# Kernel tuning notes

Measured on AMD Instinct MI355X. Metric: run time of the kernel, lower is better.

Reference implementation:

```python
import jax, jax.numpy as jnp
import numpy as np
import math

B, S, H = 2, 2048, 1024
NH, HD = 16, 64
MAX_SCALE = 4


def setup_inputs() -> dict:
    key = jax.random.key(0)
    ks = jax.random.split(key, 8)
    s = 0.02
    return {
        "x": jax.random.normal(ks[0], (B, S, H), dtype=jnp.float32),
        "Wqkv": jax.random.normal(ks[1], (H, 3 * H), dtype=jnp.float32) * s,
        "bqkv": jnp.zeros((3 * H,), dtype=jnp.float32),
        "Wout": jax.random.normal(ks[2], (H, H), dtype=jnp.float32) * s,
        "bout": jnp.zeros((H,), dtype=jnp.float32),
        "Wscale": jax.random.normal(ks[3], (H, MAX_SCALE), dtype=jnp.float32) * s,
        "bscale": jnp.zeros((MAX_SCALE,), dtype=jnp.float32),
    }


def reference(x, Wqkv, bqkv, Wout, bout, Wscale, bscale):
    b, s, h = x.shape
    inv_sqrt_hd = 1.0 / math.sqrt(HD)
    # qkv projection -> [3, b, nh, s, hd]
    qkv = (x @ Wqkv + bqkv).reshape(b, s, 3, NH, HD).transpose(2, 0, 3, 1, 4)
    q, k, v = qkv[0], qkv[1], qkv[2]
    # per-token soft weights over scales [b, s, max_scale]
    scale_weights = jax.nn.softmax(x @ Wscale + bscale, axis=-1)
    out = jnp.zeros((b, NH, s, HD), dtype=x.dtype)
    for scale_idx in range(MAX_SCALE):
        dilation = 2 ** scale_idx
        kd = k[:, :, ::dilation]  # strided (dilated) gather of keys
        vd = v[:, :, ::dilation]
        scores = jnp.einsum("bhqd,bhkd->bhqk", q, kd) * inv_sqrt_hd
        attn = jax.nn.softmax(scores, axis=-1)
        o = jnp.einsum("bhqk,bhkd->bhqd", attn, vd)
        w = scale_weights[:, :, scale_idx][:, None, :, None]  # [b,1,s,1]
        out = out + o * w
    out = out.transpose(0, 2, 1, 3).reshape(b, s, h)
    return out @ Wout + bout
```

## Files before the change

kernel.cpp:

```cpp
#include <hip/hip_runtime.h>
#include <stdint.h>

typedef unsigned short u16;
typedef __attribute__((ext_vector_type(8))) __bf16 bf8v;
typedef __attribute__((ext_vector_type(4))) float f4v;
typedef __attribute__((ext_vector_type(16))) float f16v;
typedef __attribute__((ext_vector_type(4))) uint32_t u32x4;

#define BB 2
#define SS 2048
#define HH 1024

#define OFF_Q   0u
#define OFF_K0  8388608u
#define OFF_V0  24117248u
#define OFF_WQT 39845888u
#define OFF_WOT 46137344u
#define OFF_XB  48234496u
#define OFF_SCW 56623104u

__device__ __forceinline__ u16 f2bf(float f) {
    union { float f; uint32_t u; } v; v.f = f;
    uint32_t r = v.u + 0x7fffu + ((v.u >> 16) & 1u);
    return (u16)(r >> 16);
}
__device__ __forceinline__ uint32_t pk2(float a, float b) {
    return (uint32_t)f2bf(a) | ((uint32_t)f2bf(b) << 16);
}
__device__ __forceinline__ uint32_t pkt2(float a, float b) {
    union { float f; uint32_t u; } x, y; x.f = a; y.f = b;
    return (x.u >> 16) | (y.u & 0xffff0000u);
}
__device__ __forceinline__ bf8v u2b(uint4 v) {
    union { uint4 u; bf8v b; } x; x.u = v; return x.b;
}

__global__ __launch_bounds__(256) void xconv_kernel(const float* __restrict__ x,
                                                    u16* __restrict__ xb) {
    size_t t = (size_t)blockIdx.x * 256 + threadIdx.x;
    float4 v = *(const float4*)&x[t * 4];
    uint2 pk; pk.x = pk2(v.x, v.y); pk.y = pk2(v.z, v.w);
    *(uint2*)&xb[t * 4] = pk;
}

__global__ __launch_bounds__(256) void wconv_kernel(const float* __restrict__ W,
                                                    u16* __restrict__ Wt,
                                                    int N, int K) {
    __shared__ float tile[64][69];
    const int tid = threadIdx.x;
    const int n0 = blockIdx.x * 64, k0 = blockIdx.y * 64;
    const int r = tid >> 4, c4 = (tid & 15) * 4;
#pragma unroll
    for (int it = 0; it < 4; it++) {
        float4 v = *(const float4*)&W[(size_t)(k0 + it * 16 + r) * N + n0 + c4];
        tile[it * 16 + r][c4 + 0] = v.x; tile[it * 16 + r][c4 + 1] = v.y;
        tile[it * 16 + r][c4 + 2] = v.z; tile[it * 16 + r][c4 + 3] = v.w;
    }
    __syncthreads();
#pragma unroll
    for (int it = 0; it < 4; it++) {
        int n = it * 16 + r;
        uint2 pk;
        pk.x = pk2(tile[c4 + 0][n], tile[c4 + 1][n]);
        pk.y = pk2(tile[c4 + 2][n], tile[c4 + 3][n]);
        *(uint2*)&Wt[(size_t)(n0 + n) * K + k0 + c4] = pk;
    }
}

__global__ __launch_bounds__(256) void scale_kernel(const float* __restrict__ x,
                                                    const float* __restrict__ Wscale,
                                                    const float* __restrict__ bscale,
                                                    float* __restrict__ scw) {
    const int lane = threadIdx.x & 63;
    const int wid  = threadIdx.x >> 6;
    const int row  = blockIdx.x * 4 + wid;
    float a0 = 0.f, a1 = 0.f, a2 = 0.f, a3 = 0.f;
    for (int i = 0; i < 16; i++) {
        int hh = lane + i * 64;
        float xs = x[(size_t)row * HH + hh];
        float4 wv = *(const float4*)&Wscale[hh * 4];
        a0 += xs * wv.x; a1 += xs * wv.y; a2 += xs * wv.z; a3 += xs * wv.w;
    }
    for (int off = 1; off < 64; off <<= 1) {
        a0 += __shfl_xor(a0, off); a1 += __shfl_xor(a1, off);
        a2 += __shfl_xor(a2, off); a3 += __shfl_xor(a3, off);
    }
    if (lane == 0) {
        a0 += bscale[0]; a1 += bscale[1]; a2 += bscale[2]; a3 += bscale[3];
        float mx = fmaxf(fmaxf(a0, a1), fmaxf(a2, a3));
        float e0 = __expf(a0 - mx), e1 = __expf(a1 - mx);
        float e2 = __expf(a2 - mx), e3 = __expf(a3 - mx);
        float inv = 1.f / (e0 + e1 + e2 + e3);
        float4 o = {e0 * inv, e1 * inv, e2 * inv, e3 * inv};
        *(float4*)&scw[(size_t)row * 4] = o;
    }
}

template<int MODE>
__global__ __launch_bounds__(256) void gemm_bt(const u16* __restrict__ A,
                                               const u16* __restrict__ Bt,
                                               const float* __restrict__ bias,
                                               void* __restrict__ Cp,
                                               int N, int K) {
    __shared__ __align__(16) u16 At[128 * 40];
    __shared__ __align__(16) u16 Btl[128 * 40];
    const int tid  = threadIdx.x;
    const int lane = tid & 63;
    const int wid  = tid >> 6;
    const int l15  = lane & 15;
    const int quad = lane >> 4;
    const int wm = wid & 1, wn = wid >> 1;
    const int m0 = blockIdx.y * 128;
    const int n0 = blockIdx.x * 128;
    const int srow = tid >> 2;
    const int sc8  = (tid & 3) * 8;

    f4v acc[4][4];
#pragma unroll
    for (int i = 0; i < 4; i++)
#pragma unroll
        for (int j = 0; j < 4; j++) acc[i][j] = (f4v){0.f, 0.f, 0.f, 0.f};

    uint4 pa0 = *(const uint4*)(A  + (size_t)(m0 + srow) * K + sc8);
    uint4 pa1 = *(const uint4*)(A  + (size_t)(m0 + srow + 64) * K + sc8);
    uint4 pb0 = *(const uint4*)(Bt + (size_t)(n0 + srow) * K + sc8);
    uint4 pb1 = *(const uint4*)(Bt + (size_t)(n0 + srow + 64) * K + sc8);

    for (int kc = 0; kc < K; kc += 32) {
        __syncthreads();
        *(uint4*)&At[srow * 40 + sc8]         = pa0;
        *(uint4*)&At[(srow + 64) * 40 + sc8]  = pa1;
        *(uint4*)&Btl[srow * 40 + sc8]        = pb0;
        *(uint4*)&Btl[(srow + 64) * 40 + sc8] = pb1;
        __syncthreads();
        if (kc + 32 < K) {
            pa0 = *(const uint4*)(A  + (size_t)(m0 + srow) * K + kc + 32 + sc8);
            pa1 = *(const uint4*)(A  + (size_t)(m0 + srow + 64) * K + kc + 32 + sc8);
            pb0 = *(const uint4*)(Bt + (size_t)(n0 + srow) * K + kc + 32 + sc8);
            pb1 = *(const uint4*)(Bt + (size_t)(n0 + srow + 64) * K + kc + 32 + sc8);
        }
        bf8v af[4], bf[4];
#pragma unroll
        for (int t = 0; t < 4; t++) {
            af[t] = *(const bf8v*)&At[(wm * 64 + t * 16 + l15) * 40 + quad * 8];
            bf[t] = *(const bf8v*)&Btl[(wn * 64 + t * 16 + l15) * 40 + quad * 8];
        }
#pragma unroll
        for (int ti = 0; ti < 4; ti++)
#pragma unroll
            for (int tj = 0; tj < 4; tj++)
                acc[ti][tj] = __builtin_amdgcn_mfma_f32_16x16x32_bf16(af[ti], bf[tj], acc[ti][tj], 0, 0, 0);
    }

    if (MODE == 0) {
#pragma unroll
        for (int ti = 0; ti < 4; ti++)
#pragma unroll
            for (int tj = 0; tj < 4; tj++)
#pragma unroll
                for (int r = 0; r < 4; r++) {
                    int m = m0 + wm * 64 + ti * 16 + quad * 4 + r;
                    int n = n0 + wn * 64 + tj * 16 + l15;
                    ((float*)Cp)[(size_t)m * N + n] = acc[ti][tj][r] + bias[n];
                }
    } else {
        char* ws = (char*)Cp;
        u16* Qd = (u16*)ws;
        u16* K0 = (u16*)(ws + OFF_K0);
        u16* V0 = (u16*)(ws + OFF_V0);
        const int region = n0 >> 10;
        if (region == 0) {
#pragma unroll
            for (int ti = 0; ti < 4; ti++)
#pragma unroll
                for (int tj = 0; tj < 4; tj++)
#pragma unroll
                    for (int r = 0; r < 4; r++) {
                        int m = m0 + wm * 64 + ti * 16 + quad * 4 + r;
                        int n = n0 + wn * 64 + tj * 16 + l15;
                        Qd[(size_t)m * 1024 + n] = f2bf(acc[ti][tj][r] + bias[n]);
                    }
        } else if (region == 1) {
#pragma unroll
            for (int ti = 0; ti < 4; ti++)
#pragma unroll
                for (int tj = 0; tj < 4; tj++) {
                    int n  = n0 + wn * 64 + tj * 16 + l15;
                    int nk = n - 1024;
                    int h = nk >> 6, hd = nk & 63;
#pragma unroll
                    for (int r = 0; r < 4; r++) {
                        int m = m0 + wm * 64 + ti * 16 + quad * 4 + r;
                        int bb = m >> 11, tok = m & 2047;
                        int bh = bb * 16 + h;
                        u16 bv = f2bf((acc[ti][tj][r] + bias[n]) * 0.18033688f);
                        K0[((size_t)bh * 2048 + tok) * 64 + hd] = bv;
                    }
                }
        } else {
#pragma unroll
            for (int ti = 0; ti < 4; ti++)
#pragma unroll
                for (int tj = 0; tj < 4; tj++) {
                    int n  = n0 + wn * 64 + tj * 16 + l15;
                    int nv = n - 2048;
                    int h = nv >> 6, hd = nv & 63;
                    int tokb = m0 + wm * 64 + ti * 16 + quad * 4;
                    int bb = tokb >> 11, tok = tokb & 2047;
                    int bh = bb * 16 + h;
                    float v0 = acc[ti][tj][0] + bias[n];
                    float v1 = acc[ti][tj][1] + bias[n];
                    float v2 = acc[ti][tj][2] + bias[n];
                    float v3 = acc[ti][tj][3] + bias[n];
                    u16 c0 = f2bf(v0), c1 = f2bf(v1), c2 = f2bf(v2), c3 = f2bf(v3);
                    uint2 pk;
                    pk.x = (uint32_t)c0 | ((uint32_t)c1 << 16);
                    pk.y = (uint32_t)c2 | ((uint32_t)c3 << 16);
                    int tokp = (tok & ~15) | ((tok & 4) << 1) | ((tok & 8) >> 1);
                    *(uint2*)&V0[((size_t)bh * 64 + hd) * 2048 + tokp] = pk;
                }
        }
    }
}

#define PITER(C, KA, BUFC, BUFN)                                               \
    {                                                                          \
        const int c = (C);                                                     \
        f16v sa = sinit;                                                       \
        sa = __builtin_amdgcn_mfma_f32_32x32x16_bf16(u2b(KA[0]), qf[0], sa, 0, 0, 0); \
        sa = __builtin_amdgcn_mfma_f32_32x32x16_bf16(u2b(KA[1]), qf[1], sa, 0, 0, 0); \
        sa = __builtin_amdgcn_mfma_f32_32x32x16_bf16(u2b(KA[2]), qf[2], sa, 0, 0, 0); \
        sa = __builtin_amdgcn_mfma_f32_32x32x16_bf16(u2b(KA[3]), qf[3], sa, 0, 0, 0); \
        if (c + 2 < 64) {                                                      \
            _Pragma("unroll")                                                  \
            for (int ks = 0; ks < 4; ks++)                                     \
                KA[ks] = *(const uint4*)(Kb + (size_t)((c + 2) * 32 + l31) * 64 + ks * 16 + half * 8); \
        }                                                                      \
        if (c + 1 < 64) *(uint4*)&(BUFN)[sr * 40 + svk8] = vr;                 \
        if (c + 2 < 64) vr = *(const uint4*)(Vb0 + (size_t)sr * 2048 + (c + 2) * 32 + svk8); \
        uint32_t F0, F1, F2, F3, F4, F5, F6, F7;                               \
        {                                                                      \
            float x0, x1, x2, x3;                                              \
            x0 = exp2f(sa[0]);  x1 = exp2f(sa[1]);                             \
            x2 = exp2f(sa[2]);  x3 = exp2f(sa[3]);                             \
            F0 = pkt2(x0, x1); F1 = pkt2(x2, x3);                              \
            x0 = exp2f(sa[4]);  x1 = exp2f(sa[5]);                             \
            x2 = exp2f(sa[6]);  x3 = exp2f(sa[7]);                             \
            F2 = pkt2(x0, x1); F3 = pkt2(x2, x3);                              \
            x0 = exp2f(sa[8]);  x1 = exp2f(sa[9]);                             \
            x2 = exp2f(sa[10]); x3 = exp2f(sa[11]);                            \
            F4 = pkt2(x0, x1); F5 = pkt2(x2, x3);                              \
            x0 = exp2f(sa[12]); x1 = exp2f(sa[13]);                            \
            x2 = exp2f(sa[14]); x3 = exp2f(sa[15]);                            \
            F6 = pkt2(x0, x1); F7 = pkt2(x2, x3);                              \
        }                                                                      \
        uu p0; p0.u = (u32x4){F0, F1, F2, F3};                                 \
        uu p1; p1.u = (u32x4){F4, F5, F6, F7};                                 \
        bf8v va00 = *(const bf8v*)&(BUFC)[l31 * 40 + half * 8];                \
        oacc[0] = __builtin_amdgcn_mfma_f32_32x32x16_bf16(va00, p0.b, oacc[0], 0, 0, 0); \
        bf8v va01 = *(const bf8v*)&(BUFC)[l31 * 40 + 16 + half * 8];           \
        oacc[0] = __builtin_amdgcn_mfma_f32_32x32x16_bf16(va01, p1.b, oacc[0], 0, 0, 0); \
        bf8v va10 = *(const bf8v*)&(BUFC)[(32 + l31) * 40 + half * 8];         \
        oacc[1] = __builtin_amdgcn_mfma_f32_32x32x16_bf16(va10, p0.b, oacc[1], 0, 0, 0); \
        bf8v va11 = *(const bf8v*)&(BUFC)[(32 + l31) * 40 + 16 + half * 8];    \
        oacc[1] = __builtin_amdgcn_mfma_f32_32x32x16_bf16(va11, p1.b, oacc[1], 0, 0, 0); \
        __syncthreads();                                                       \
    }

__global__ __launch_bounds__(256, 2) void attn_kernel(const char* __restrict__ ws) {
    __shared__ __align__(16) u16 smem[5120];
    u16* Vt0 = smem;
    u16* Vt1 = smem + 2560;

    const u16* Qd    = (const u16*)(ws + OFF_Q);
    const float* scw = (const float*)(ws + OFF_SCW);
    u16* attnb       = (u16*)(ws + OFF_Q);

    const int tid  = threadIdx.x;
    const int lane = tid & 63;
    const int wid  = tid >> 6;
    const int l31  = lane & 31;
    const int half = lane >> 5;

    const int f   = blockIdx.x + 16 * blockIdx.y + 256 * blockIdx.z;
    const int xcd = f & 7, jj = f >> 3;
    const int grp = xcd * 4 + (jj >> 4);
    const int qt  = jj & 15;
    const int b = grp >> 4, h = grp & 15;
    const int q  = qt * 128 + wid * 32 + l31;
    const int bh = b * 16 + h;

    const int sr   = tid >> 2;
    const int svk8 = (tid & 3) * 8;

    bf8v qf[4];
#pragma unroll
    for (int ks = 0; ks < 4; ks++)
        qf[ks] = *(const bf8v*)(Qd + (size_t)(b * SS + q) * 1024 + h * 64 + ks * 16 + half * 8);

    const u16* Kb  = (const u16*)(ws + OFF_K0) + (size_t)bh * (2048 * 64);
    const u16* Vb0 = (const u16*)(ws + OFF_V0) + (size_t)bh * (64 * 2048);

    union uu { u32x4 u; bf8v b; };

    float ls0 = 0.f, ls1 = 0.f, ls2 = 0.f, ls3 = 0.f;
    uint4 kp[4], kq[4];
#pragma unroll
    for (int ks = 0; ks < 4; ks++) {
        kp[ks] = *(const uint4*)(Kb + (size_t)l31 * 64 + ks * 16 + half * 8);
        kq[ks] = *(const uint4*)(Kb + (size_t)(32 + l31) * 64 + ks * 16 + half * 8);
    }
    for (int c = 0; c < 64; c += 2) {
        f16v sA = {0,0,0,0,0,0,0,0,0,0,0,0,0,0,0,0};
        f16v sB = {0,0,0,0,0,0,0,0,0,0,0,0,0,0,0,0};
#pragma unroll
        for (int ks = 0; ks < 4; ks++) {
            sA = __builtin_amdgcn_mfma_f32_32x32x16_bf16(u2b(kp[ks]), qf[ks], sA, 0, 0, 0);
            sB = __builtin_amdgcn_mfma_f32_32x32x16_bf16(u2b(kq[ks]), qf[ks], sB, 0, 0, 0);
        }
        if (c + 2 < 64) {
#pragma unroll
            for (int ks = 0; ks < 4; ks++)
                kp[ks] = *(const uint4*)(Kb + (size_t)((c + 2) * 32 + l31) * 64 + ks * 16 + half * 8);
#pragma unroll
            for (int ks = 0; ks < 4; ks++)
                kq[ks] = *(const uint4*)(Kb + (size_t)((c + 3) * 32 + l31) * 64 + ks * 16 + half * 8);
        }
#pragma unroll
        for (int g = 0; g < 4; g++) {
            float x0 = exp2f(sA[4 * g + 0]);
            float x1 = exp2f(sA[4 * g + 1]);
            float x2 = exp2f(sA[4 * g + 2]);
            float x3 = exp2f(sA[4 * g + 3]);
            ls0 += (x0 + x1) + (x2 + x3);
            ls1 += x0 + x2;
            ls2 += x0;
            if (!half) ls3 += x0;
        }
#pragma unroll
        for (int g = 0; g < 4; g++) {
            float x0 = exp2f(sB[4 * g + 0]);
            float x1 = exp2f(sB[4 * g + 1]);
            float x2 = exp2f(sB[4 * g + 2]);
            float x3 = exp2f(sB[4 * g + 3]);
            ls0 += (x0 + x1) + (x2 + x3);
            ls1 += x0 + x2;
            ls2 += x0;
            if (!half) ls3 += x0;
        }
    }
    ls0 += __shfl_xor(ls0, 32);
    ls1 += __shfl_xor(ls1, 32);
    ls2 += __shfl_xor(ls2, 32);
    ls3 += __shfl_xor(ls3, 32);

    float4 sw = *(const float4*)&scw[(size_t)(b * SS + q) * 4];
    float m0v = sw.x / ls0;
    float m2v = m0v + sw.y / ls1;
    float mAv = m2v + sw.z / ls2;
    float mBv = mAv + sw.w / ls3;
    float lmO = log2f(m0v);
    float lmE = log2f(m2v);
    float lmZ = log2f(half ? mAv : mBv);
    f16v sinit;
#pragma unroll
    for (int g = 0; g < 4; g++) {
        sinit[4 * g + 0] = lmZ; sinit[4 * g + 1] = lmO;
        sinit[4 * g + 2] = lmE; sinit[4 * g + 3] = lmO;
    }

    f16v oacc[2];
#pragma unroll
    for (int ht = 0; ht < 2; ht++)
#pragma unroll
        for (int r = 0; r < 16; r++) oacc[ht][r] = 0.f;

    *(uint4*)&Vt0[sr * 40 + svk8] = *(const uint4*)(Vb0 + (size_t)sr * 2048 + svk8);
    uint4 vr = *(const uint4*)(Vb0 + (size_t)sr * 2048 + 32 + svk8);
#pragma unroll
    for (int ks = 0; ks < 4; ks++) {
        kp[ks] = *(const uint4*)(Kb + (size_t)l31 * 64 + ks * 16 + half * 8);
        kq[ks] = *(const uint4*)(Kb + (size_t)(32 + l31) * 64 + ks * 16 + half * 8);
    }
    __syncthreads();

    for (int cc = 0; cc < 64; cc += 2) {
        PITER(cc,     kp, Vt0, Vt1)
        PITER(cc + 1, kq, Vt1, Vt0)
    }

    const size_t base = (size_t)(b * SS + q) * 1024 + h * 64;
#pragma unroll
    for (int ht = 0; ht < 2; ht++)
#pragma unroll
        for (int g = 0; g < 4; g++) {
            uint2 pk;
            pk.x = pk2(oacc[ht][g * 4 + 0], oacc[ht][g * 4 + 1]);
            pk.y = pk2(oacc[ht][g * 4 + 2], oacc[ht][g * 4 + 3]);
            *(uint2*)&attnb[base + ht * 32 + g * 8 + half * 4] = pk;
        }
}

extern "C" void kernel_launch(void* const* d_in, const int* in_sizes, int n_in,
                              void* d_out, int out_size, void* d_ws, size_t ws_size,
                              hipStream_t stream) {
    const float* x      = (const float*)d_in[0];
    const float* Wqkv   = (const float*)d_in[1];
    const float* bqkv   = (const float*)d_in[2];
    const float* Wout   = (const float*)d_in[3];
    const float* bout   = (const float*)d_in[4];
    const float* Wscale = (const float*)d_in[5];
    const float* bscale = (const float*)d_in[6];
    float* out = (float*)d_out;

    char* ws = (char*)d_ws;
    u16*   wqt   = (u16*)(ws + OFF_WQT);
    u16*   wot   = (u16*)(ws + OFF_WOT);
    u16*   xb    = (u16*)(ws + OFF_XB);
    u16*   attnb = (u16*)(ws + OFF_Q);
    float* scw   = (float*)(ws + OFF_SCW);

    xconv_kernel<<<dim3(4096), dim3(256), 0, stream>>>(x, xb);
    wconv_kernel<<<dim3(48, 16), dim3(256), 0, stream>>>(Wqkv, wqt, 3072, 1024);
    wconv_kernel<<<dim3(16, 16), dim3(256), 0, stream>>>(Wout, wot, 1024, 1024);
    scale_kernel<<<dim3(1024), dim3(256), 0, stream>>>(x, Wscale, bscale, scw);
    gemm_bt<1><<<dim3(24, 32), dim3(256), 0, stream>>>(xb, wqt, bqkv, (void*)ws, 3072, 1024);
    attn_kernel<<<dim3(16, 16, 2), dim3(256), 0, stream>>>(ws);
    gemm_bt<0><<<dim3(8, 32), dim3(256), 0, stream>>>(attnb, wot, bout, (void*)out, 1024, 1024);
}
```

Measured before the change: 284.1 us.

## Split attention key range across two wave groups and reduce via LDS

Doubles the attention block to 512 threads so two groups of four waves each process half of the key sequence, for both the normalizer pass and the output pass. Partial row sums and partial output accumulators are combined through shared memory before the final write. The shared-memory V double-buffer and its per-chunk block barriers are removed, and V fragments are read directly from global memory. This is meant to raise occupancy and parallelism, at the cost of uncoalesced direct V loads, no software prefetch of K, and extra reduction traffic.

```diff
diff --git a/kernel.cpp b/kernel.cpp
--- a/kernel.cpp
+++ b/kernel.cpp
@@ -223,54 +223,8 @@
     }
 }
 
-#define PITER(C, KA, BUFC, BUFN)                                               \
-    {                                                                          \
-        const int c = (C);                                                     \
-        f16v sa = sinit;                                                       \
-        sa = __builtin_amdgcn_mfma_f32_32x32x16_bf16(u2b(KA[0]), qf[0], sa, 0, 0, 0); \
-        sa = __builtin_amdgcn_mfma_f32_32x32x16_bf16(u2b(KA[1]), qf[1], sa, 0, 0, 0); \
-        sa = __builtin_amdgcn_mfma_f32_32x32x16_bf16(u2b(KA[2]), qf[2], sa, 0, 0, 0); \
-        sa = __builtin_amdgcn_mfma_f32_32x32x16_bf16(u2b(KA[3]), qf[3], sa, 0, 0, 0); \
-        if (c + 2 < 64) {                                                      \
-            _Pragma("unroll")                                                  \
-            for (int ks = 0; ks < 4; ks++)                                     \
-                KA[ks] = *(const uint4*)(Kb + (size_t)((c + 2) * 32 + l31) * 64 + ks * 16 + half * 8); \
-        }                                                                      \
-        if (c + 1 < 64) *(uint4*)&(BUFN)[sr * 40 + svk8] = vr;                 \
-        if (c + 2 < 64) vr = *(const uint4*)(Vb0 + (size_t)sr * 2048 + (c + 2) * 32 + svk8); \
-        uint32_t F0, F1, F2, F3, F4, F5, F6, F7;                               \
-        {                                                                      \
-            float x0, x1, x2, x3;                                              \
-            x0 = exp2f(sa[0]);  x1 = exp2f(sa[1]);                             \
-            x2 = exp2f(sa[2]);  x3 = exp2f(sa[3]);                             \
-            F0 = pkt2(x0, x1); F1 = pkt2(x2, x3);                              \
-            x0 = exp2f(sa[4]);  x1 = exp2f(sa[5]);                             \
-            x2 = exp2f(sa[6]);  x3 = exp2f(sa[7]);                             \
-            F2 = pkt2(x0, x1); F3 = pkt2(x2, x3);                              \
-            x0 = exp2f(sa[8]);  x1 = exp2f(sa[9]);                             \
-            x2 = exp2f(sa[10]); x3 = exp2f(sa[11]);                            \
-            F4 = pkt2(x0, x1); F5 = pkt2(x2, x3);                              \
-            x0 = exp2f(sa[12]); x1 = exp2f(sa[13]);                            \
-            x2 = exp2f(sa[14]); x3 = exp2f(sa[15]);                            \
-            F6 = pkt2(x0, x1); F7 = pkt2(x2, x3);                              \
-        }                                                                      \
-        uu p0; p0.u = (u32x4){F0, F1, F2, F3};                                 \
-        uu p1; p1.u = (u32x4){F4, F5, F6, F7};                                 \
-        bf8v va00 = *(const bf8v*)&(BUFC)[l31 * 40 + half * 8];                \
-        oacc[0] = __builtin_amdgcn_mfma_f32_32x32x16_bf16(va00, p0.b, oacc[0], 0, 0, 0); \
-        bf8v va01 = *(const bf8v*)&(BUFC)[l31 * 40 + 16 + half * 8];           \
-        oacc[0] = __builtin_amdgcn_mfma_f32_32x32x16_bf16(va01, p1.b, oacc[0], 0, 0, 0); \
-        bf8v va10 = *(const bf8v*)&(BUFC)[(32 + l31) * 40 + half * 8];         \
-        oacc[1] = __builtin_amdgcn_mfma_f32_32x32x16_bf16(va10, p0.b, oacc[1], 0, 0, 0); \
-        bf8v va11 = *(const bf8v*)&(BUFC)[(32 + l31) * 40 + 16 + half * 8];    \
-        oacc[1] = __builtin_amdgcn_mfma_f32_32x32x16_bf16(va11, p1.b, oacc[1], 0, 0, 0); \
-        __syncthreads();                                                       \
-    }
-
-__global__ __launch_bounds__(256, 2) void attn_kernel(const char* __restrict__ ws) {
-    __shared__ __align__(16) u16 smem[5120];
-    u16* Vt0 = smem;
-    u16* Vt1 = smem + 2560;
+__global__ __launch_bounds__(512, 4) void attn_kernel(const char* __restrict__ ws) {
+    __shared__ __align__(16) float smemf[8192];
 
     const u16* Qd    = (const u16*)(ws + OFF_Q);
     const float* scw = (const float*)(ws + OFF_SCW);
@@ -279,6 +233,8 @@
     const int tid  = threadIdx.x;
     const int lane = tid & 63;
     const int wid  = tid >> 6;
+    const int wq   = wid & 3;
+    const int sp   = wid >> 2;
     const int l31  = lane & 31;
     const int half = lane >> 5;
 
@@ -287,72 +243,81 @@
     const int grp = xcd * 4 + (jj >> 4);
     const int qt  = jj & 15;
     const int b = grp >> 4, h = grp & 15;
-    const int q  = qt * 128 + wid * 32 + l31;
+    const int q  = qt * 128 + wq * 32 + l31;
     const int bh = b * 16 + h;
-
-    const int sr   = tid >> 2;
-    const int svk8 = (tid & 3) * 8;
 
     bf8v qf[4];
 #pragma unroll
     for (int ks = 0; ks < 4; ks++)
         qf[ks] = *(const bf8v*)(Qd + (size_t)(b * SS + q) * 1024 + h * 64 + ks * 16 + half * 8);
 
-    const u16* Kb  = (const u16*)(ws + OFF_K0) + (size_t)bh * (2048 * 64);
-    const u16* Vb0 = (const u16*)(ws + OFF_V0) + (size_t)bh * (64 * 2048);
+    const u16* Kb  = (const u16*)(ws + OFF_K0) + (size_t)bh * (2048 * 64) + (size_t)(sp * 1024) * 64;
+    const u16* Vb0 = (const u16*)(ws + OFF_V0) + (size_t)bh * (64 * 2048) + (size_t)(sp * 1024);
 
     union uu { u32x4 u; bf8v b; };
 
     float ls0 = 0.f, ls1 = 0.f, ls2 = 0.f, ls3 = 0.f;
-    uint4 kp[4], kq[4];
-#pragma unroll
-    for (int ks = 0; ks < 4; ks++) {
-        kp[ks] = *(const uint4*)(Kb + (size_t)l31 * 64 + ks * 16 + half * 8);
-        kq[ks] = *(const uint4*)(Kb + (size_t)(32 + l31) * 64 + ks * 16 + half * 8);
-    }
-    for (int c = 0; c < 64; c += 2) {
-        f16v sA = {0,0,0,0,0,0,0,0,0,0,0,0,0,0,0,0};
-        f16v sB = {0,0,0,0,0,0,0,0,0,0,0,0,0,0,0,0};
+    {
+        uint4 kp[4], kq[4];
 #pragma unroll
         for (int ks = 0; ks < 4; ks++) {
-            sA = __builtin_amdgcn_mfma_f32_32x32x16_bf16(u2b(kp[ks]), qf[ks], sA, 0, 0, 0);
-            sB = __builtin_amdgcn_mfma_f32_32x32x16_bf16(u2b(kq[ks]), qf[ks], sB, 0, 0, 0);
-        }
-        if (c + 2 < 64) {
-#pragma unroll
-            for (int ks = 0; ks < 4; ks++)
-                kp[ks] = *(const uint4*)(Kb + (size_t)((c + 2) * 32 + l31) * 64 + ks * 16 + half * 8);
-#pragma unroll
-            for (int ks = 0; ks < 4; ks++)
-                kq[ks] = *(const uint4*)(Kb + (size_t)((c + 3) * 32 + l31) * 64 + ks * 16 + half * 8);
-        }
-#pragma unroll
-        for (int g = 0; g < 4; g++) {
-            float x0 = exp2f(sA[4 * g + 0]);
-            float x1 = exp2f(sA[4 * g + 1]);
-            float x2 = exp2f(sA[4 * g + 2]);
-            float x3 = exp2f(sA[4 * g + 3]);
-            ls0 += (x0 + x1) + (x2 + x3);
-            ls1 += x0 + x2;
-            ls2 += x0;
-            if (!half) ls3 += x0;
-        }
-#pragma unroll
-        for (int g = 0; g < 4; g++) {
-            float x0 = exp2f(sB[4 * g + 0]);
-            float x1 = exp2f(sB[4 * g + 1]);
-            float x2 = exp2f(sB[4 * g + 2]);
-            float x3 = exp2f(sB[4 * g + 3]);
-            ls0 += (x0 + x1) + (x2 + x3);
-            ls1 += x0 + x2;
-            ls2 += x0;
-            if (!half) ls3 += x0;
+            kp[ks] = *(const uint4*)(Kb + (size_t)l31 * 64 + ks * 16 + half * 8);
+            kq[ks] = *(const uint4*)(Kb + (size_t)(32 + l31) * 64 + ks * 16 + half * 8);
+        }
+        for (int c = 0; c < 32; c += 2) {
+            f16v sA = {0,0,0,0,0,0,0,0,0,0,0,0,0,0,0,0};
+            f16v sB = {0,0,0,0,0,0,0,0,0,0,0,0,0,0,0,0};
+#pragma unroll
+            for (int ks = 0; ks < 4; ks++) {
+                sA = __builtin_amdgcn_mfma_f32_32x32x16_bf16(u2b(kp[ks]), qf[ks], sA, 0, 0, 0);
+                sB = __builtin_amdgcn_mfma_f32_32x32x16_bf16(u2b(kq[ks]), qf[ks], sB, 0, 0, 0);
+            }
+            if (c + 2 < 32) {
+#pragma unroll
+                for (int ks = 0; ks < 4; ks++)
+                    kp[ks] = *(const uint4*)(Kb + (size_t)((c + 2) * 32 + l31) * 64 + ks * 16 + half * 8);
+#pragma unroll
+                for (int ks = 0; ks < 4; ks++)
+                    kq[ks] = *(const uint4*)(Kb + (size_t)((c + 3) * 32 + l31) * 64 + ks * 16 + half * 8);
+            }
+#pragma unroll
+            for (int g = 0; g < 4; g++) {
+                float x0 = exp2f(sA[4 * g + 0]);
+                float x1 = exp2f(sA[4 * g + 1]);
+                float x2 = exp2f(sA[4 * g + 2]);
+                float x3 = exp2f(sA[4 * g + 3]);
+                ls0 += (x0 + x1) + (x2 + x3);
+                ls1 += x0 + x2;
+                ls2 += x0;
+                if (!half) ls3 += x0;
+            }
+#pragma unroll
+            for (int g = 0; g < 4; g++) {
+                float x0 = exp2f(sB[4 * g + 0]);
+                float x1 = exp2f(sB[4 * g + 1]);
+                float x2 = exp2f(sB[4 * g + 2]);
+                float x3 = exp2f(sB[4 * g + 3]);
+                ls0 += (x0 + x1) + (x2 + x3);
+                ls1 += x0 + x2;
+                ls2 += x0;
+                if (!half) ls3 += x0;
+            }
         }
     }
     ls0 += __shfl_xor(ls0, 32);
     ls1 += __shfl_xor(ls1, 32);
     ls2 += __shfl_xor(ls2, 32);
     ls3 += __shfl_xor(ls3, 32);
+
+    if (!half) {
+        float4 mine = {ls0, ls1, ls2, ls3};
+        ((float4*)smemf)[wid * 32 + l31] = mine;
+    }
+    __syncthreads();
+    {
+        float4 oth = ((float4*)smemf)[(wid ^ 4) * 32 + l31];
+        ls0 += oth.x; ls1 += oth.y; ls2 += oth.z; ls3 += oth.w;
+    }
 
     float4 sw = *(const float4*)&scw[(size_t)(b * SS + q) * 4];
     float m0v = sw.x / ls0;
@@ -368,6 +333,7 @@
         sinit[4 * g + 0] = lmZ; sinit[4 * g + 1] = lmO;
         sinit[4 * g + 2] = lmE; sinit[4 * g + 3] = lmO;
     }
+    __syncthreads();
 
     f16v oacc[2];
 #pragma unroll
@@ -375,30 +341,71 @@
 #pragma unroll
         for (int r = 0; r < 16; r++) oacc[ht][r] = 0.f;
 
-    *(uint4*)&Vt0[sr * 40 + svk8] = *(const uint4*)(Vb0 + (size_t)sr * 2048 + svk8);
-    uint4 vr = *(const uint4*)(Vb0 + (size_t)sr * 2048 + 32 + svk8);
-#pragma unroll
-    for (int ks = 0; ks < 4; ks++) {
-        kp[ks] = *(const uint4*)(Kb + (size_t)l31 * 64 + ks * 16 + half * 8);
-        kq[ks] = *(const uint4*)(Kb + (size_t)(32 + l31) * 64 + ks * 16 + half * 8);
+    for (int c = 0; c < 32; c++) {
+        uint4 kf[4];
+#pragma unroll
+        for (int ks = 0; ks < 4; ks++)
+            kf[ks] = *(const uint4*)(Kb + (size_t)(c * 32 + l31) * 64 + ks * 16 + half * 8);
+        f16v sa = sinit;
+#pragma unroll
+        for (int ks = 0; ks < 4; ks++)
+            sa = __builtin_amdgcn_mfma_f32_32x32x16_bf16(u2b(kf[ks]), qf[ks], sa, 0, 0, 0);
+
+        uint32_t F0, F1, F2, F3, F4, F5, F6, F7;
+        {
+            float x0, x1, x2, x3;
+            x0 = exp2f(sa[0]);  x1 = exp2f(sa[1]);
+            x2 = exp2f(sa[2]);  x3 = exp2f(sa[3]);
+            F0 = pkt2(x0, x1); F1 = pkt2(x2, x3);
+            x0 = exp2f(sa[4]);  x1 = exp2f(sa[5]);
+            x2 = exp2f(sa[6]);  x3 = exp2f(sa[7]);
+            F2 = pkt2(x0, x1); F3 = pkt2(x2, x3);
+            x0 = exp2f(sa[8]);  x1 = exp2f(sa[9]);
+            x2 = exp2f(sa[10]); x3 = exp2f(sa[11]);
+            F4 = pkt2(x0, x1); F5 = pkt2(x2, x3);
+            x0 = exp2f(sa[12]); x1 = exp2f(sa[13]);
+            x2 = exp2f(sa[14]); x3 = exp2f(sa[15]);
+            F6 = pkt2(x0, x1); F7 = pkt2(x2, x3);
+        }
+        uu p0; p0.u = (u32x4){F0, F1, F2, F3};
+        uu p1; p1.u = (u32x4){F4, F5, F6, F7};
+        {
+            bf8v va00 = *(const bf8v*)(Vb0 + (size_t)l31 * 2048 + c * 32 + half * 8);
+            oacc[0] = __builtin_amdgcn_mfma_f32_32x32x16_bf16(va00, p0.b, oacc[0], 0, 0, 0);
+            bf8v va01 = *(const bf8v*)(Vb0 + (size_t)l31 * 2048 + c * 32 + 16 + half * 8);
+            oacc[0] = __builtin_amdgcn_mfma_f32_32x32x16_bf16(va01, p1.b, oacc[0], 0, 0, 0);
+            bf8v va10 = *(const bf8v*)(Vb0 + (size_t)(32 + l31) * 2048 + c * 32 + half * 8);
+            oacc[1] = __builtin_amdgcn_mfma_f32_32x32x16_bf16(va10, p0.b, oacc[1], 0, 0, 0);
+            bf8v va11 = *(const bf8v*)(Vb0 + (size_t)(32 + l31) * 2048 + c * 32 + 16 + half * 8);
+            oacc[1] = __builtin_amdgcn_mfma_f32_32x32x16_bf16(va11, p1.b, oacc[1], 0, 0, 0);
+        }
+    }
+
+    if (sp == 1) {
+#pragma unroll
+        for (int ht = 0; ht < 2; ht++)
+#pragma unroll
+            for (int r = 0; r < 16; r++)
+                smemf[wq * 2048 + (ht * 16 + r) * 64 + lane] = oacc[ht][r];
     }
     __syncthreads();
-
-    for (int cc = 0; cc < 64; cc += 2) {
-        PITER(cc,     kp, Vt0, Vt1)
-        PITER(cc + 1, kq, Vt1, Vt0)
-    }
-
-    const size_t base = (size_t)(b * SS + q) * 1024 + h * 64;
-#pragma unroll
-    for (int ht = 0; ht < 2; ht++)
-#pragma unroll
-        for (int g = 0; g < 4; g++) {
-            uint2 pk;
-            pk.x = pk2(oacc[ht][g * 4 + 0], oacc[ht][g * 4 + 1]);
-            pk.y = pk2(oacc[ht][g * 4 + 2], oacc[ht][g * 4 + 3]);
-            *(uint2*)&attnb[base + ht * 32 + g * 8 + half * 4] = pk;
-        }
+    if (sp == 0) {
+#pragma unroll
+        for (int ht = 0; ht < 2; ht++)
+#pragma unroll
+            for (int r = 0; r < 16; r++)
+                oacc[ht][r] += smemf[wq * 2048 + (ht * 16 + r) * 64 + lane];
+        const size_t base = (size_t)(b * SS + q) * 1024 + h * 64;
+#pragma unroll
+        for (int ht = 0; ht < 2; ht++)
+#pragma unroll
+            for (int g = 0; g < 4; g++) {
+                uint2 pk;
+                pk.x = pk2(oacc[ht][g * 4 + 0], oacc[ht][g * 4 + 1]);
+                pk.y = pk2(oacc[ht][g * 4 + 2], oacc[ht][g * 4 + 3]);
+                *(uint2*)&attnb[base + ht * 32 + g * 8 + half * 4] = pk;
+            }
+    }
 }
 
 extern "C" void kernel_launch(void* const* d_in, const int* in_sizes, int n_in,
@@ -425,6 +432,6 @@
     wconv_kernel<<<dim3(16, 16), dim3(256), 0, stream>>>(Wout, wot, 1024, 1024);
     scale_kernel<<<dim3(1024), dim3(256), 0, stream>>>(x, Wscale, bscale, scw);
     gemm_bt<1><<<dim3(24, 32), dim3(256), 0, stream>>>(xb, wqt, bqkv, (void*)ws, 3072, 1024);
-    attn_kernel<<<dim3(16, 16, 2), dim3(256), 0, stream>>>(ws);
+    attn_kernel<<<dim3(16, 16, 2), dim3(512), 0, stream>>>(ws);
     gemm_bt<0><<<dim3(8, 32), dim3(256), 0, stream>>>(attnb, wot, bout, (void*)out, 1024, 1024);
 }
```

New measurement: 334.9 us. 17.9% more time.
